# Optimization experiments

Measured on AMD Instinct MI355X. Metric: run time of the kernel, lower is better.

The kernel has to match this reference:

```python
import jax, jax.numpy as jnp
import numpy as np

B, LQ, LKV = 2, 512, 4096
Q_DIM = KV_DIM = QK_OUT = V_OUT = OUT_DIM = 512
H = 8
E = 10
TOPK = 5
QK_HEAD = QK_OUT // H
V_HEAD = V_OUT // H
SCALE = 1.0 / (QK_HEAD ** 0.5)


def _moe_params(key, in_dim, out_dim):
    k1, k2, k3, k4 = jax.random.split(key, 4)
    s = 0.02
    return (
        jax.random.normal(k1, (in_dim, E), dtype=jnp.float32) * s,   # gate W
        jax.random.normal(k2, (E,), dtype=jnp.float32) * s,          # gate b
        jax.random.normal(k3, (E, in_dim, out_dim), dtype=jnp.float32) * s,  # expert W
        jax.random.normal(k4, (E, out_dim), dtype=jnp.float32) * s,  # expert b
    )


def setup_inputs() -> dict:
    key = jax.random.key(0)
    ks = jax.random.split(key, 6)
    q = jax.random.normal(ks[0], (B, LQ, Q_DIM), dtype=jnp.float32)
    kv = jax.random.normal(ks[1], (B, LKV, KV_DIM), dtype=jnp.float32)
    q_gw, q_gb, q_w, q_b = _moe_params(ks[2], Q_DIM, QK_OUT)
    k_gw, k_gb, k_w, k_b = _moe_params(ks[3], KV_DIM, QK_OUT)
    v_gw, v_gb, v_w, v_b = _moe_params(ks[4], KV_DIM, V_OUT)
    o_gw, o_gb, o_w, o_b = _moe_params(ks[5], V_OUT, OUT_DIM)
    return {
        'q': q, 'kv': kv,
        'q_gw': q_gw, 'q_gb': q_gb, 'q_w': q_w, 'q_b': q_b,
        'k_gw': k_gw, 'k_gb': k_gb, 'k_w': k_w, 'k_b': k_b,
        'v_gw': v_gw, 'v_gb': v_gb, 'v_w': v_w, 'v_b': v_b,
        'o_gw': o_gw, 'o_gb': o_gb, 'o_w': o_w, 'o_b': o_b,
    }


def moe_linear(x, gw, gb, W, b, top_k=TOPK):
    # gate: softmax over experts, then keep top-k and renormalize
    gate = jax.nn.softmax(x @ gw + gb, axis=-1)            # [B,S,E]
    topv, idx = jax.lax.top_k(gate, top_k)                 # [B,S,k]
    oneh = jax.nn.one_hot(idx, E, dtype=gate.dtype)        # [B,S,k,E]
    g = jnp.einsum('bsk,bske->bse', topv, oneh)
    g = g / g.sum(-1, keepdims=True)
    # dense compute of all experts, then gate-weighted sum (faithful to source)
    y = jnp.einsum('bsi,eio->bsoe', x, W) + b.T            # [B,S,O,E]
    return jnp.einsum('bsoe,bse->bso', y, g)


def reference(q, kv, q_gw, q_gb, q_w, q_b, k_gw, k_gb, k_w, k_b,
              v_gw, v_gb, v_w, v_b, o_gw, o_gb, o_w, o_b):
    qp = moe_linear(q, q_gw, q_gb, q_w, q_b)               # [B,LQ,QK_OUT]
    kp = moe_linear(kv, k_gw, k_gb, k_w, k_b)              # [B,LKV,QK_OUT]
    vp = moe_linear(kv, v_gw, v_gb, v_w, v_b)              # [B,LKV,V_OUT]
    qh = qp.reshape(B, LQ, H, QK_HEAD).transpose(0, 2, 1, 3)
    kh = kp.reshape(B, LKV, H, QK_HEAD).transpose(0, 2, 1, 3)
    vh = vp.reshape(B, LKV, H, V_HEAD).transpose(0, 2, 1, 3)
    attn = jnp.einsum('bhqd,bhkd->bhqk', qh, kh) * SCALE   # [B,H,LQ,LKV]
    attn = jax.nn.softmax(attn, axis=-1)                   # no mask, dropout=0 (eval)
    x = jnp.einsum('bhqk,bhkd->bhqd', attn, vh)
    x = x.transpose(0, 2, 1, 3).reshape(B, LQ, V_OUT)
    x = moe_linear(x, o_gw, o_gb, o_w, o_b)                # out_proj (also MoE, top_k=5)
    return x, attn
```

## Files before the change

### kernel.cpp

```cpp
#include <hip/hip_runtime.h>
#include <hip/hip_bf16.h>

typedef __bf16 bf16_t;
typedef __bf16 bf16x8 __attribute__((ext_vector_type(8)));
typedef __bf16 bf16x4 __attribute__((ext_vector_type(4)));
typedef float f32x4 __attribute__((ext_vector_type(4)));

#define NE 10
#define DM 512
#define SCALE_F 0.125f

__device__ __forceinline__ void gl16(const void* g, void* l) {
    __builtin_amdgcn_global_load_lds(
        (const __attribute__((address_space(1))) unsigned int*)g,
        (__attribute__((address_space(3))) unsigned int*)l, 16, 0, 0);
}

__global__ void cast_bf16_kernel(const float* __restrict__ in, bf16_t* __restrict__ out, int n)
{
    const int i = (blockIdx.x * 256 + threadIdx.x) * 8;
    if (i >= n) return;
    float4 a = *(const float4*)(in + i);
    float4 b = *(const float4*)(in + i + 4);
    bf16x8 o;
    o[0] = (bf16_t)a.x; o[1] = (bf16_t)a.y; o[2] = (bf16_t)a.z; o[3] = (bf16_t)a.w;
    o[4] = (bf16_t)b.x; o[5] = (bf16_t)b.y; o[6] = (bf16_t)b.z; o[7] = (bf16_t)b.w;
    *(bf16x8*)(out + i) = o;
}

__global__ void wtrans4_kernel(const float* __restrict__ W0, const float* __restrict__ W1,
                               const float* __restrict__ W2, const float* __restrict__ W3,
                               bf16_t* __restrict__ Wt)
{
    __shared__ float tile[32][33];
    const int z = blockIdx.z, which = z / NE, e = z - which * NE;
    const float* W = which == 0 ? W0 : which == 1 ? W1 : which == 2 ? W2 : W3;
    const int n0 = blockIdx.x * 32, k0 = blockIdx.y * 32;
    const int tx = threadIdx.x & 31, ty = threadIdx.x >> 5;
    const float* Wp = W + ((size_t)e * DM + k0) * DM + n0;
#pragma unroll
    for (int r = 0; r < 32; r += 8) tile[ty + r][tx] = Wp[(size_t)(ty + r) * DM + tx];
    __syncthreads();
    bf16_t* Op = Wt + (((size_t)which * NE + e) * DM + n0) * DM + k0;
#pragma unroll
    for (int r = 0; r < 32; r += 8) Op[(size_t)(ty + r) * DM + tx] = (bf16_t)tile[tx][ty + r];
}

__device__ __forceinline__ void topk_write(const float* p, const float* __restrict__ gb,
                                           float* __restrict__ G, int t)
{
    float l[NE], ex[NE];
    float mx = -3.4e38f;
#pragma unroll
    for (int e = 0; e < NE; e++) { l[e] = p[e] + gb[e]; mx = fmaxf(mx, l[e]); }
#pragma unroll
    for (int e = 0; e < NE; e++) ex[e] = __expf(l[e] - mx);
    bool sel[NE];
#pragma unroll
    for (int e = 0; e < NE; e++) sel[e] = false;
    float ssel = 0.f;
    for (int j = 0; j < 5; j++) {
        int bi = 0; float bv = -3.4e38f;
        for (int e = 0; e < NE; e++)
            if (!sel[e] && l[e] > bv) { bv = l[e]; bi = e; }
        sel[bi] = true; ssel += ex[bi];
    }
    const float inv = 1.f / ssel;
    for (int e = 0; e < NE; e++) G[(size_t)t * NE + e] = sel[e] ? ex[e] * inv : 0.f;
}

__global__ void moe_gates(const float* __restrict__ X, const float* __restrict__ gw,
                          const float* __restrict__ gb, float* __restrict__ G)
{
    const int t = blockIdx.x;
    const int lane = threadIdx.x;
    const float* x = X + (size_t)t * DM;
    float p[NE];
#pragma unroll
    for (int e = 0; e < NE; e++) p[e] = 0.f;
    for (int i = lane; i < DM; i += 64) {
        const float xv = x[i];
        const float* g = gw + (size_t)i * NE;
#pragma unroll
        for (int e = 0; e < NE; e++) p[e] += xv * g[e];
    }
#pragma unroll
    for (int off = 32; off > 0; off >>= 1)
#pragma unroll
        for (int e = 0; e < NE; e++) p[e] += __shfl_down(p[e], off);
    if (lane == 0) topk_write(p, gb, G, t);
}

__global__ void moe_gates_kv(const float* __restrict__ X,
                             const float* __restrict__ kgw, const float* __restrict__ kgb,
                             const float* __restrict__ vgw, const float* __restrict__ vgb,
                             float* __restrict__ Gk, float* __restrict__ Gv)
{
    const int t = blockIdx.x * 4 + (threadIdx.x >> 6);
    const int lane = threadIdx.x & 63;
    const float* x = X + (size_t)t * DM;
    float xr[8];
    *(float4*)&xr[0] = *(const float4*)(x + lane * 8);
    *(float4*)&xr[4] = *(const float4*)(x + lane * 8 + 4);
    float pk[NE], pv[NE];
#pragma unroll
    for (int e = 0; e < NE; e++) { pk[e] = 0.f; pv[e] = 0.f; }
#pragma unroll
    for (int j = 0; j < 8; j++) {
        const int i = lane * 8 + j;
        const float* gk = kgw + (size_t)i * NE;
        const float* gv = vgw + (size_t)i * NE;
#pragma unroll
        for (int e = 0; e < NE; e++) { pk[e] += xr[j] * gk[e]; pv[e] += xr[j] * gv[e]; }
    }
#pragma unroll
    for (int off = 32; off > 0; off >>= 1)
#pragma unroll
        for (int e = 0; e < NE; e++) { pk[e] += __shfl_down(pk[e], off); pv[e] += __shfl_down(pv[e], off); }
    if (lane == 0) { topk_write(pk, kgb, Gk, t); topk_write(pv, vgb, Gv, t); }
}

__global__ void gate_bias_init(const float* __restrict__ G, const float* __restrict__ b,
                               float* __restrict__ out)
{
    const int idx = blockIdx.x * 256 + threadIdx.x;
    const int t = idx >> 9, n = idx & 511;
    const float* g = G + (size_t)t * NE;
    float s = 0.f;
#pragma unroll
    for (int e = 0; e < NE; e++) s += g[e] * b[e * DM + n];
    out[idx] = s;
}

__global__ __launch_bounds__(256, 2)
void moe_gemm_kv(const bf16_t* __restrict__ X,
                 const bf16_t* __restrict__ Wk, const bf16_t* __restrict__ Wv,
                 const float* __restrict__ kb, const float* __restrict__ vb,
                 const float* __restrict__ Gk, const float* __restrict__ Gv,
                 bf16_t* __restrict__ kp, bf16_t* __restrict__ vpT)
{
    constexpr int BM = 128, BN = 128, BK = 64;
    __shared__ bf16_t As[BM * BK];
    __shared__ bf16_t Bs[BN * BK];
    __shared__ float Gs[BM][NE];
    __shared__ float BiasS[NE][BN];

    const int tid = threadIdx.x, lane = tid & 63, w = tid >> 6;
    const int wr = w >> 1, wc = w & 1;
    const int l15 = lane & 15, quad = lane >> 4;
    const int fl = blockIdx.y * 64 + blockIdx.x;
    const int nfl = ((fl & 7) << 6) | (fl >> 3);
    const int bx = nfl & 63, by = nfl >> 6;
    const int m0 = bx * BM;
    const int side = by >> 2;
    const int n0 = (by & 3) * BN;
    const bf16_t* Wt = side ? Wv : Wk;
    const float* G = side ? Gv : Gk;
    const float* bias = side ? vb : kb;

    for (int i = tid; i < BM * NE; i += 256) {
        int r = i / NE, e = i - r * NE;
        Gs[r][e] = G[(size_t)(m0 + r) * NE + e];
    }
    for (int i = tid; i < NE * BN; i += 256) {
        int e = i / BN, j = i - e * BN;
        BiasS[e][j] = bias[(size_t)e * DM + n0 + j];
    }

    const int rsub = lane >> 3, pch = lane & 7, csw = pch ^ rsub;
    const bf16_t* aptr[4]; bf16_t* alds[4]; bf16_t* blds[4];
#pragma unroll
    for (int j = 0; j < 4; j++) {
        const int rb = w * 32 + j * 8;
        aptr[j] = X + (size_t)(m0 + rb + rsub) * DM + csw * 8;
        alds[j] = (bf16_t*)As + rb * BK;
        blds[j] = (bf16_t*)Bs + rb * BK;
    }
    int amr[4], bnr[4];
#pragma unroll
    for (int f = 0; f < 4; f++) { amr[f] = wr * 64 + f * 16 + l15; bnr[f] = wc * 64 + f * 16 + l15; }

    const f32x4 zv = {0.f, 0.f, 0.f, 0.f};
    f32x4 acc[4][4];
#pragma unroll
    for (int a = 0; a < 4; a++)
#pragma unroll
        for (int c = 0; c < 4; c++) acc[a][c] = zv;

    for (int e = 0; e < NE; e++) {
        const bf16_t* bbase = Wt + ((size_t)e * DM + n0 + w * 32 + rsub) * DM + csw * 8;
        f32x4 acc2[4][4];
#pragma unroll
        for (int a = 0; a < 4; a++)
#pragma unroll
            for (int c = 0; c < 4; c++) acc2[a][c] = zv;

        for (int kt = 0; kt < 8; kt++) {
            __syncthreads();
#pragma unroll
            for (int j = 0; j < 4; j++) gl16(aptr[j] + kt * BK, alds[j]);
#pragma unroll
            for (int j = 0; j < 4; j++) gl16(bbase + (size_t)j * 8 * DM + kt * BK, blds[j]);
            __syncthreads();
#pragma unroll
            for (int kss = 0; kss < 2; kss++) {
                bf16x8 af[4], bfv[4];
#pragma unroll
                for (int f = 0; f < 4; f++) {
                    af[f]  = *(const bf16x8*)(As + amr[f] * BK + (((kss << 2) | quad) ^ (amr[f] & 7)) * 8);
                    bfv[f] = *(const bf16x8*)(Bs + bnr[f] * BK + (((kss << 2) | quad) ^ (bnr[f] & 7)) * 8);
                }
#pragma unroll
                for (int mf = 0; mf < 4; mf++)
#pragma unroll
                    for (int nf = 0; nf < 4; nf++)
                        acc2[mf][nf] = __builtin_amdgcn_mfma_f32_16x16x32_bf16(
                            af[mf], bfv[nf], acc2[mf][nf], 0, 0, 0);
            }
        }
#pragma unroll
        for (int mf = 0; mf < 4; mf++)
#pragma unroll
            for (int r = 0; r < 4; r++) {
                const float g = Gs[wr * 64 + mf * 16 + quad * 4 + r][e];
#pragma unroll
                for (int nf = 0; nf < 4; nf++) acc[mf][nf][r] += g * acc2[mf][nf][r];
            }
    }

#pragma unroll
    for (int mf = 0; mf < 4; mf++) {
#pragma unroll
        for (int nf = 0; nf < 4; nf++) {
            const int n = wc * 64 + nf * 16 + l15;
            float vals[4];
#pragma unroll
            for (int r = 0; r < 4; r++) {
                const int m = wr * 64 + mf * 16 + quad * 4 + r;
                float v = acc[mf][nf][r];
#pragma unroll
                for (int e = 0; e < NE; e++) v += Gs[m][e] * BiasS[e][n];
                vals[r] = v;
            }
            if (side) {
                const int mg = m0 + wr * 64 + mf * 16 + quad * 4;
                const int b = mg >> 12, t = mg & 4095;
                bf16x4 pk;
                pk[0] = (bf16_t)vals[0]; pk[1] = (bf16_t)vals[1];
                pk[2] = (bf16_t)vals[2]; pk[3] = (bf16_t)vals[3];
                *(bf16x4*)(vpT + ((size_t)(b * DM) + n0 + n) * 4096 + t) = pk;
            } else {
#pragma unroll
                for (int r = 0; r < 4; r++) {
                    const int m = wr * 64 + mf * 16 + quad * 4 + r;
                    kp[(size_t)(m0 + m) * DM + n0 + n] = (bf16_t)vals[r];
                }
            }
        }
    }
}

__global__ __launch_bounds__(256, 4)
void moe_gemm_split(const bf16_t* __restrict__ X, const bf16_t* __restrict__ Wt,
                    const float* __restrict__ G, float* __restrict__ out)
{
    constexpr int BK = 64;
    __shared__ bf16_t As[64 * BK];
    __shared__ bf16_t Bs[64 * BK];
    __shared__ float Gs[64][2];
    const int tid = threadIdx.x, lane = tid & 63, w = tid >> 6;
    const int wr = w >> 1, wc = w & 1;
    const int l15 = lane & 15, quad = lane >> 4;
    const int fl = blockIdx.z * 128 + blockIdx.y * 16 + blockIdx.x;
    const int nfl = (fl & 7) * 80 + (fl >> 3);
    const int bx = nfl & 15, by = (nfl >> 4) & 7, bz = nfl >> 7;
    const int m0 = bx * 64, n0 = by * 64, e0 = bz * 2;

    if (tid < 128) {
        int r = tid >> 1, e = tid & 1;
        Gs[r][e] = G[(size_t)(m0 + r) * NE + e0 + e];
    }

    const int rsub = lane >> 3, pch = lane & 7, csw = pch ^ rsub;
    const bf16_t* aptr[2]; bf16_t* alds[2]; bf16_t* blds[2];
#pragma unroll
    for (int j = 0; j < 2; j++) {
        const int rb = w * 16 + j * 8;
        aptr[j] = X + (size_t)(m0 + rb + rsub) * DM + csw * 8;
        alds[j] = (bf16_t*)As + rb * BK;
        blds[j] = (bf16_t*)Bs + rb * BK;
    }
    const int amr[2] = {wr * 32 + l15, wr * 32 + 16 + l15};
    const int bnr[2] = {wc * 32 + l15, wc * 32 + 16 + l15};

    const f32x4 zv = {0.f, 0.f, 0.f, 0.f};
    f32x4 acc[2][2];
#pragma unroll
    for (int a = 0; a < 2; a++)
#pragma unroll
        for (int c = 0; c < 2; c++) acc[a][c] = zv;

#pragma unroll
    for (int ee = 0; ee < 2; ee++) {
        const int e = e0 + ee;
        const bf16_t* bbase = Wt + ((size_t)e * DM + n0 + w * 16 + rsub) * DM + csw * 8;
        f32x4 acc2[2][2];
#pragma unroll
        for (int a = 0; a < 2; a++)
#pragma unroll
            for (int c = 0; c < 2; c++) acc2[a][c] = zv;
        for (int kt = 0; kt < 8; kt++) {
            __syncthreads();
#pragma unroll
            for (int j = 0; j < 2; j++) gl16(aptr[j] + kt * BK, alds[j]);
#pragma unroll
            for (int j = 0; j < 2; j++) gl16(bbase + (size_t)j * 8 * DM + kt * BK, blds[j]);
            __syncthreads();
#pragma unroll
            for (int kss = 0; kss < 2; kss++) {
                bf16x8 af[2], bfv[2];
#pragma unroll
                for (int f = 0; f < 2; f++) {
                    af[f]  = *(const bf16x8*)(As + amr[f] * BK + (((kss << 2) | quad) ^ (amr[f] & 7)) * 8);
                    bfv[f] = *(const bf16x8*)(Bs + bnr[f] * BK + (((kss << 2) | quad) ^ (bnr[f] & 7)) * 8);
                }
#pragma unroll
                for (int mf = 0; mf < 2; mf++)
#pragma unroll
                    for (int nf = 0; nf < 2; nf++)
                        acc2[mf][nf] = __builtin_amdgcn_mfma_f32_16x16x32_bf16(
                            af[mf], bfv[nf], acc2[mf][nf], 0, 0, 0);
            }
        }
#pragma unroll
        for (int mf = 0; mf < 2; mf++)
#pragma unroll
            for (int r = 0; r < 4; r++) {
                const float g = Gs[wr * 32 + mf * 16 + quad * 4 + r][ee];
#pragma unroll
                for (int nf = 0; nf < 2; nf++) acc[mf][nf][r] += g * acc2[mf][nf][r];
            }
    }
#pragma unroll
    for (int mf = 0; mf < 2; mf++)
#pragma unroll
        for (int nf = 0; nf < 2; nf++) {
            const int n = n0 + wc * 32 + nf * 16 + l15;
#pragma unroll
            for (int r = 0; r < 4; r++) {
                const int m = m0 + wr * 32 + mf * 16 + quad * 4 + r;
                atomicAdd(&out[(size_t)m * DM + n], acc[mf][nf][r]);
            }
        }
}

__global__ __launch_bounds__(256, 2)
void attn_pass1(const float* __restrict__ qp, const bf16_t* __restrict__ kp,
                float* __restrict__ mws, float* __restrict__ lws)
{
    __shared__ bf16_t Qs[64][72];
    __shared__ bf16_t Ks[64 * 64];
    const int fl = (blockIdx.z << 5) | (blockIdx.y << 2) | blockIdx.x;
    const int nfl = ((fl & 7) << 6) | (fl >> 3);
    const int ksp = nfl & 3, qt = (nfl >> 2) & 7, bh = nfl >> 5;
    const int b = bh >> 3, h = bh & 7, q0 = qt * 64;
    const int tid = threadIdx.x, lane = tid & 63, w = tid >> 6;
    const int l15 = lane & 15, quad = lane >> 4;

    {
        const int row = tid >> 2, cg = (tid & 3) * 16;
        const float* qs = qp + ((size_t)(b * 512 + q0 + row)) * DM + h * 64 + cg;
        float4 f[4];
#pragma unroll
        for (int j = 0; j < 4; j++) f[j] = *(const float4*)(qs + j * 4);
        bf16x8 o0, o1;
        o0[0]=(bf16_t)(f[0].x*SCALE_F); o0[1]=(bf16_t)(f[0].y*SCALE_F); o0[2]=(bf16_t)(f[0].z*SCALE_F); o0[3]=(bf16_t)(f[0].w*SCALE_F);
        o0[4]=(bf16_t)(f[1].x*SCALE_F); o0[5]=(bf16_t)(f[1].y*SCALE_F); o0[6]=(bf16_t)(f[1].z*SCALE_F); o0[7]=(bf16_t)(f[1].w*SCALE_F);
        o1[0]=(bf16_t)(f[2].x*SCALE_F); o1[1]=(bf16_t)(f[2].y*SCALE_F); o1[2]=(bf16_t)(f[2].z*SCALE_F); o1[3]=(bf16_t)(f[2].w*SCALE_F);
        o1[4]=(bf16_t)(f[3].x*SCALE_F); o1[5]=(bf16_t)(f[3].y*SCALE_F); o1[6]=(bf16_t)(f[3].z*SCALE_F); o1[7]=(bf16_t)(f[3].w*SCALE_F);
        *(bf16x8*)&Qs[row][cg] = o0;
        *(bf16x8*)&Qs[row][cg + 8] = o1;
    }
    const int rsub = lane >> 3, pch = lane & 7, csw = pch ^ rsub;
    const bf16_t* kptr[2]; bf16_t* klds[2];
#pragma unroll
    for (int j = 0; j < 2; j++) {
        const int rb = w * 16 + j * 8;
        kptr[j] = kp + ((size_t)(b * 4096 + rb + rsub)) * DM + h * 64 + csw * 8;
        klds[j] = (bf16_t*)Ks + rb * 64;
    }
    float mrun[4], lrun[4];
#pragma unroll
    for (int r = 0; r < 4; r++) { mrun[r] = -3.0e38f; lrun[r] = 0.f; }

    for (int kt = 0; kt < 16; kt++) {
        const size_t koff = (size_t)(ksp * 16 + kt) * 64 * DM;
        __syncthreads();
        gl16(kptr[0] + koff, klds[0]);
        gl16(kptr[1] + koff, klds[1]);
        __syncthreads();
        const f32x4 zv = {0.f, 0.f, 0.f, 0.f};
        f32x4 sacc[4] = {zv, zv, zv, zv};
#pragma unroll
        for (int kss = 0; kss < 2; kss++) {
            bf16x8 af = *(const bf16x8*)&Qs[w * 16 + l15][kss * 32 + quad * 8];
#pragma unroll
            for (int nf = 0; nf < 4; nf++) {
                const int br = nf * 16 + l15;
                bf16x8 bfv = *(const bf16x8*)(Ks + br * 64 + (((kss << 2) | quad) ^ (br & 7)) * 8);
                sacc[nf] = __builtin_amdgcn_mfma_f32_16x16x32_bf16(af, bfv, sacc[nf], 0, 0, 0);
            }
        }
#pragma unroll
        for (int r = 0; r < 4; r++) {
            float tm = fmaxf(fmaxf(sacc[0][r], sacc[1][r]), fmaxf(sacc[2][r], sacc[3][r]));
#pragma unroll
            for (int off = 1; off < 16; off <<= 1) tm = fmaxf(tm, __shfl_xor(tm, off));
            const float mn = fmaxf(mrun[r], tm);
            float s = __expf(sacc[0][r] - mn) + __expf(sacc[1][r] - mn) +
                      __expf(sacc[2][r] - mn) + __expf(sacc[3][r] - mn);
#pragma unroll
            for (int off = 1; off < 16; off <<= 1) s += __shfl_xor(s, off);
            lrun[r] = lrun[r] * __expf(mrun[r] - mn) + s;
            mrun[r] = mn;
        }
    }
    if (l15 == 0) {
#pragma unroll
        for (int r = 0; r < 4; r++) {
            const int row = q0 + w * 16 + quad * 4 + r;
            mws[((size_t)ksp * 16 + bh) * 512 + row] = mrun[r];
            lws[((size_t)ksp * 16 + bh) * 512 + row] = lrun[r];
        }
    }
}

__global__ __launch_bounds__(256, 2)
void attn_pass2(const float* __restrict__ qp, const bf16_t* __restrict__ kp,
                const bf16_t* __restrict__ vpT, const float* __restrict__ mws,
                const float* __restrict__ lws, float* __restrict__ attn,
                float* __restrict__ xout)
{
    __shared__ bf16_t Qs[64][72];
    __shared__ bf16_t Ks[64 * 64];
    __shared__ bf16_t Vs[64 * 64];
    __shared__ bf16_t Ps[64][72];
    const int fl = (blockIdx.z << 5) | (blockIdx.y << 2) | blockIdx.x;
    const int nfl = ((fl & 7) << 6) | (fl >> 3);
    const int ksp = nfl & 3, qt = (nfl >> 2) & 7, bh = nfl >> 5;
    const int b = bh >> 3, h = bh & 7, q0 = qt * 64;
    const int tid = threadIdx.x, lane = tid & 63, w = tid >> 6;
    const int l15 = lane & 15, quad = lane >> 4;

    {
        const int row = tid >> 2, cg = (tid & 3) * 16;
        const float* qs = qp + ((size_t)(b * 512 + q0 + row)) * DM + h * 64 + cg;
        float4 f[4];
#pragma unroll
        for (int j = 0; j < 4; j++) f[j] = *(const float4*)(qs + j * 4);
        bf16x8 o0, o1;
        o0[0]=(bf16_t)(f[0].x*SCALE_F); o0[1]=(bf16_t)(f[0].y*SCALE_F); o0[2]=(bf16_t)(f[0].z*SCALE_F); o0[3]=(bf16_t)(f[0].w*SCALE_F);
        o0[4]=(bf16_t)(f[1].x*SCALE_F); o0[5]=(bf16_t)(f[1].y*SCALE_F); o0[6]=(bf16_t)(f[1].z*SCALE_F); o0[7]=(bf16_t)(f[1].w*SCALE_F);
        o1[0]=(bf16_t)(f[2].x*SCALE_F); o1[1]=(bf16_t)(f[2].y*SCALE_F); o1[2]=(bf16_t)(f[2].z*SCALE_F); o1[3]=(bf16_t)(f[2].w*SCALE_F);
        o1[4]=(bf16_t)(f[3].x*SCALE_F); o1[5]=(bf16_t)(f[3].y*SCALE_F); o1[6]=(bf16_t)(f[3].z*SCALE_F); o1[7]=(bf16_t)(f[3].w*SCALE_F);
        *(bf16x8*)&Qs[row][cg] = o0;
        *(bf16x8*)&Qs[row][cg + 8] = o1;
    }
    float mrow[4], linv[4];
#pragma unroll
    for (int r = 0; r < 4; r++) {
        const int row = q0 + w * 16 + quad * 4 + r;
        float mv[4], lv[4], mm = -3.0e38f;
#pragma unroll
        for (int p = 0; p < 4; p++) {
            mv[p] = mws[((size_t)p * 16 + bh) * 512 + row];
            lv[p] = lws[((size_t)p * 16 + bh) * 512 + row];
            mm = fmaxf(mm, mv[p]);
        }
        float ll = 0.f;
#pragma unroll
        for (int p = 0; p < 4; p++) ll += lv[p] * __expf(mv[p] - mm);
        mrow[r] = mm; linv[r] = 1.f / ll;
    }
    const int rsub = lane >> 3, pch = lane & 7, csw = pch ^ rsub;
    const bf16_t* kptr[2]; const bf16_t* vptr[2]; bf16_t* klds[2]; bf16_t* vlds[2];
#pragma unroll
    for (int j = 0; j < 2; j++) {
        const int rb = w * 16 + j * 8;
        kptr[j] = kp + ((size_t)(b * 4096 + rb + rsub)) * DM + h * 64 + csw * 8;
        vptr[j] = vpT + ((size_t)(b * DM + h * 64 + rb + rsub)) * 4096 + csw * 8;
        klds[j] = (bf16_t*)Ks + rb * 64;
        vlds[j] = (bf16_t*)Vs + rb * 64;
    }
    const f32x4 zv = {0.f, 0.f, 0.f, 0.f};
    f32x4 oacc[4] = {zv, zv, zv, zv};
    float* ap = attn + ((size_t)bh * 512) * 4096;

    for (int kt = 0; kt < 16; kt++) {
        const int kg = (ksp * 16 + kt) * 64;
        __syncthreads();
        gl16(kptr[0] + (size_t)kg * DM, klds[0]);
        gl16(kptr[1] + (size_t)kg * DM, klds[1]);
        gl16(vptr[0] + kg, vlds[0]);
        gl16(vptr[1] + kg, vlds[1]);
        __syncthreads();
        f32x4 sacc[4] = {zv, zv, zv, zv};
#pragma unroll
        for (int kss = 0; kss < 2; kss++) {
            bf16x8 af = *(const bf16x8*)&Qs[w * 16 + l15][kss * 32 + quad * 8];
#pragma unroll
            for (int nf = 0; nf < 4; nf++) {
                const int br = nf * 16 + l15;
                bf16x8 bfv = *(const bf16x8*)(Ks + br * 64 + (((kss << 2) | quad) ^ (br & 7)) * 8);
                sacc[nf] = __builtin_amdgcn_mfma_f32_16x16x32_bf16(af, bfv, sacc[nf], 0, 0, 0);
            }
        }
#pragma unroll
        for (int nf = 0; nf < 4; nf++)
#pragma unroll
            for (int r = 0; r < 4; r++) {
                const float p = __expf(sacc[nf][r] - mrow[r]) * linv[r];
                ap[((size_t)(q0 + w * 16 + quad * 4 + r)) * 4096 + kg + nf * 16 + l15] = p;
                Ps[w * 16 + quad * 4 + r][nf * 16 + l15] = (bf16_t)p;
            }
        __syncthreads();
#pragma unroll
        for (int kss = 0; kss < 2; kss++) {
            bf16x8 paf = *(const bf16x8*)&Ps[w * 16 + l15][kss * 32 + quad * 8];
#pragma unroll
            for (int nf = 0; nf < 4; nf++) {
                const int br = nf * 16 + l15;
                bf16x8 vb = *(const bf16x8*)(Vs + br * 64 + (((kss << 2) | quad) ^ (br & 7)) * 8);
                oacc[nf] = __builtin_amdgcn_mfma_f32_16x16x32_bf16(paf, vb, oacc[nf], 0, 0, 0);
            }
        }
    }
#pragma unroll
    for (int nf = 0; nf < 4; nf++) {
        const int n = h * 64 + nf * 16 + l15;
#pragma unroll
        for (int r = 0; r < 4; r++) {
            const int m = b * 512 + q0 + w * 16 + quad * 4 + r;
            atomicAdd(&xout[(size_t)m * DM + n], oacc[nf][r]);
        }
    }
}

extern "C" void kernel_launch(void* const* d_in, const int* in_sizes, int n_in,
                              void* d_out, int out_size, void* d_ws, size_t ws_size,
                              hipStream_t stream)
{
    (void)in_sizes; (void)n_in; (void)out_size; (void)ws_size;
    const float* q    = (const float*)d_in[0];
    const float* kv   = (const float*)d_in[1];
    const float* q_gw = (const float*)d_in[2];
    const float* q_gb = (const float*)d_in[3];
    const float* q_w  = (const float*)d_in[4];
    const float* q_b  = (const float*)d_in[5];
    const float* k_gw = (const float*)d_in[6];
    const float* k_gb = (const float*)d_in[7];
    const float* k_w  = (const float*)d_in[8];
    const float* k_b  = (const float*)d_in[9];
    const float* v_gw = (const float*)d_in[10];
    const float* v_gb = (const float*)d_in[11];
    const float* v_w  = (const float*)d_in[12];
    const float* v_b  = (const float*)d_in[13];
    const float* o_gw = (const float*)d_in[14];
    const float* o_gb = (const float*)d_in[15];
    const float* o_w  = (const float*)d_in[16];
    const float* o_b  = (const float*)d_in[17];

    float* out0 = (float*)d_out;
    float* attn = out0 + (size_t)1024 * 512;

    char* ws = (char*)d_ws;
    size_t off = 0;
    auto alloc = [&](size_t bytes) {
        void* p = ws + off;
        off += (bytes + 255) & ~(size_t)255;
        return p;
    };
    bf16_t* Xq    = (bf16_t*)alloc((size_t)1024 * 512 * 2);
    bf16_t* Xkv   = (bf16_t*)alloc((size_t)8192 * 512 * 2);
    bf16_t* Wall  = (bf16_t*)alloc((size_t)4 * NE * 512 * 512 * 2);
    bf16_t* Wq_t  = Wall;
    bf16_t* Wk_t  = Wall + (size_t)1 * NE * 512 * 512;
    bf16_t* Wv_t  = Wall + (size_t)2 * NE * 512 * 512;
    bf16_t* Wo_t  = Wall + (size_t)3 * NE * 512 * 512;
    float*  qpf   = (float*)alloc((size_t)1024 * 512 * 4);
    bf16_t* kp    = (bf16_t*)alloc((size_t)8192 * 512 * 2);
    bf16_t* vpT   = (bf16_t*)alloc((size_t)8192 * 512 * 2);
    float*  xatt  = (float*)alloc((size_t)1024 * 512 * 4);
    bf16_t* xbf   = (bf16_t*)alloc((size_t)1024 * 512 * 2);
    float*  Gq    = (float*)alloc((size_t)1024 * NE * 4);
    float*  Gk    = (float*)alloc((size_t)8192 * NE * 4);
    float*  Gv    = (float*)alloc((size_t)8192 * NE * 4);
    float*  Go    = (float*)alloc((size_t)1024 * NE * 4);
    float*  mws   = (float*)alloc((size_t)4 * 16 * 512 * 4);
    float*  lws   = (float*)alloc((size_t)4 * 16 * 512 * 4);

    cast_bf16_kernel<<<256, 256, 0, stream>>>(q, Xq, 1024 * 512);
    cast_bf16_kernel<<<2048, 256, 0, stream>>>(kv, Xkv, 8192 * 512);
    wtrans4_kernel<<<dim3(16, 16, 4 * NE), 256, 0, stream>>>(q_w, k_w, v_w, o_w, Wall);
    moe_gates<<<1024, 64, 0, stream>>>(q, q_gw, q_gb, Gq);
    moe_gates_kv<<<2048, 256, 0, stream>>>(kv, k_gw, k_gb, v_gw, v_gb, Gk, Gv);

    gate_bias_init<<<2048, 256, 0, stream>>>(Gq, q_b, qpf);
    moe_gemm_split<<<dim3(16, 8, 5), 256, 0, stream>>>(Xq, Wq_t, Gq, qpf);
    moe_gemm_kv<<<dim3(64, 8), 256, 0, stream>>>(Xkv, Wk_t, Wv_t, k_b, v_b, Gk, Gv, kp, vpT);

    attn_pass1<<<dim3(4, 8, 16), 256, 0, stream>>>(qpf, kp, mws, lws);
    hipMemsetAsync(xatt, 0, (size_t)1024 * 512 * 4, stream);
    attn_pass2<<<dim3(4, 8, 16), 256, 0, stream>>>(qpf, kp, vpT, mws, lws, attn, xatt);

    moe_gates<<<1024, 64, 0, stream>>>(xatt, o_gw, o_gb, Go);
    cast_bf16_kernel<<<256, 256, 0, stream>>>(xatt, xbf, 1024 * 512);
    gate_bias_init<<<2048, 256, 0, stream>>>(Go, o_b, out0);
    moe_gemm_split<<<dim3(16, 8, 5), 256, 0, stream>>>(xbf, Wo_t, Go, out0);
}
```

Baseline: 468.5 us.

## Double-buffer LDS tiles in KV MoE GEMM to overlap loads with MFMA

Splits the A and B shared-memory tiles of the K/V MoE GEMM into two ping-pong buffers. The next K-slice, which may cross an expert boundary, is issued with global_load_lds into one buffer while MFMAs consume the other. This removes the barrier-load-barrier stall at every k-step. In exchange the kernel doubles its tile LDS use, which may limit occupancy under the two-blocks-per-CU launch bound, and the K loop is unrolled more heavily.

```diff
diff --git a/kernel.cpp b/kernel.cpp
--- a/kernel.cpp
+++ b/kernel.cpp
@@ -140,8 +140,10 @@
                  bf16_t* __restrict__ kp, bf16_t* __restrict__ vpT)
 {
     constexpr int BM = 128, BN = 128, BK = 64;
-    __shared__ bf16_t As[BM * BK];
-    __shared__ bf16_t Bs[BN * BK];
+    __shared__ bf16_t As0[BM * BK];
+    __shared__ bf16_t As1[BM * BK];
+    __shared__ bf16_t Bs0[BN * BK];
+    __shared__ bf16_t Bs1[BN * BK];
     __shared__ float Gs[BM][NE];
     __shared__ float BiasS[NE][BN];
 
@@ -168,17 +170,26 @@
     }
 
     const int rsub = lane >> 3, pch = lane & 7, csw = pch ^ rsub;
-    const bf16_t* aptr[4]; bf16_t* alds[4]; bf16_t* blds[4];
+    const bf16_t* aptr[4]; int soff[4];
 #pragma unroll
     for (int j = 0; j < 4; j++) {
         const int rb = w * 32 + j * 8;
         aptr[j] = X + (size_t)(m0 + rb + rsub) * DM + csw * 8;
-        alds[j] = (bf16_t*)As + rb * BK;
-        blds[j] = (bf16_t*)Bs + rb * BK;
-    }
+        soff[j] = rb * BK;
+    }
+    const bf16_t* wb0 = Wt + ((size_t)(n0 + w * 32 + rsub)) * DM + csw * 8;
     int amr[4], bnr[4];
 #pragma unroll
     for (int f = 0; f < 4; f++) { amr[f] = wr * 64 + f * 16 + l15; bnr[f] = wc * 64 + f * 16 + l15; }
+
+    auto stage = [&](bf16_t* Ad, bf16_t* Bd, int it) __attribute__((always_inline)) {
+        const int e_ = it >> 3, kt_ = it & 7;
+        const bf16_t* bb = wb0 + (size_t)e_ * (DM * DM) + kt_ * BK;
+#pragma unroll
+        for (int j = 0; j < 4; j++) gl16(aptr[j] + kt_ * BK, Ad + soff[j]);
+#pragma unroll
+        for (int j = 0; j < 4; j++) gl16(bb + (size_t)j * 8 * DM, Bd + soff[j]);
+    };
 
     const f32x4 zv = {0.f, 0.f, 0.f, 0.f};
     f32x4 acc[4][4];
@@ -187,28 +198,27 @@
 #pragma unroll
         for (int c = 0; c < 4; c++) acc[a][c] = zv;
 
+    stage(As0, Bs0, 0);
+    __syncthreads();
+
     for (int e = 0; e < NE; e++) {
-        const bf16_t* bbase = Wt + ((size_t)e * DM + n0 + w * 32 + rsub) * DM + csw * 8;
         f32x4 acc2[4][4];
 #pragma unroll
         for (int a = 0; a < 4; a++)
 #pragma unroll
             for (int c = 0; c < 4; c++) acc2[a][c] = zv;
 
-        for (int kt = 0; kt < 8; kt++) {
-            __syncthreads();
-#pragma unroll
-            for (int j = 0; j < 4; j++) gl16(aptr[j] + kt * BK, alds[j]);
-#pragma unroll
-            for (int j = 0; j < 4; j++) gl16(bbase + (size_t)j * 8 * DM + kt * BK, blds[j]);
-            __syncthreads();
+#pragma unroll
+        for (int kpair = 0; kpair < 4; kpair++) {
+            const int it = e * 8 + kpair * 2;
+            stage(As1, Bs1, it + 1);
 #pragma unroll
             for (int kss = 0; kss < 2; kss++) {
                 bf16x8 af[4], bfv[4];
 #pragma unroll
                 for (int f = 0; f < 4; f++) {
-                    af[f]  = *(const bf16x8*)(As + amr[f] * BK + (((kss << 2) | quad) ^ (amr[f] & 7)) * 8);
-                    bfv[f] = *(const bf16x8*)(Bs + bnr[f] * BK + (((kss << 2) | quad) ^ (bnr[f] & 7)) * 8);
+                    af[f]  = *(const bf16x8*)(As0 + amr[f] * BK + (((kss << 2) | quad) ^ (amr[f] & 7)) * 8);
+                    bfv[f] = *(const bf16x8*)(Bs0 + bnr[f] * BK + (((kss << 2) | quad) ^ (bnr[f] & 7)) * 8);
                 }
 #pragma unroll
                 for (int mf = 0; mf < 4; mf++)
@@ -217,6 +227,24 @@
                         acc2[mf][nf] = __builtin_amdgcn_mfma_f32_16x16x32_bf16(
                             af[mf], bfv[nf], acc2[mf][nf], 0, 0, 0);
             }
+            __syncthreads();
+            if (it + 2 < NE * 8) stage(As0, Bs0, it + 2);
+#pragma unroll
+            for (int kss = 0; kss < 2; kss++) {
+                bf16x8 af[4], bfv[4];
+#pragma unroll
+                for (int f = 0; f < 4; f++) {
+                    af[f]  = *(const bf16x8*)(As1 + amr[f] * BK + (((kss << 2) | quad) ^ (amr[f] & 7)) * 8);
+                    bfv[f] = *(const bf16x8*)(Bs1 + bnr[f] * BK + (((kss << 2) | quad) ^ (bnr[f] & 7)) * 8);
+                }
+#pragma unroll
+                for (int mf = 0; mf < 4; mf++)
+#pragma unroll
+                    for (int nf = 0; nf < 4; nf++)
+                        acc2[mf][nf] = __builtin_amdgcn_mfma_f32_16x16x32_bf16(
+                            af[mf], bfv[nf], acc2[mf][nf], 0, 0, 0);
+            }
+            __syncthreads();
         }
 #pragma unroll
         for (int mf = 0; mf < 4; mf++)
```

Result: slower. 510.0 us (+8.9%).
